# Performance work log

Hardware: AMD Instinct MI355X
Metric: run time of the kernel (lower is better)

The kernel has to match this reference:

```python
import jax, jax.numpy as jnp
import numpy as np

N = 50000          # nodes
E = 1600000        # edges (avg degree 32)
G = 256            # graphs in batch
IN_DIM = 128
HID = 64
NUM_LAYERS = 12    # stacked layers after the first
NUM_REL = 3
NEG_SLOPE = 0.2    # RGATConv default leaky_relu slope


def setup_inputs() -> dict:
    key = jax.random.key(0)
    ks = jax.random.split(key, 12)
    return {
        "node_features": jax.random.normal(ks[0], (N, IN_DIM), jnp.float32),
        "edge_index": jax.random.randint(ks[1], (2, E), 0, N, jnp.int32),
        "edge_type": jax.random.randint(ks[2], (E,), 0, NUM_REL, jnp.int32),
        "batch_index": jnp.sort(jax.random.randint(ks[3], (N,), 0, G, jnp.int32)),
        "W_first": jax.random.normal(ks[4], (NUM_REL, IN_DIM, HID), jnp.float32) / np.sqrt(IN_DIM).astype(np.float32),
        "q_first": jax.random.normal(ks[5], (HID,), jnp.float32) / np.sqrt(HID).astype(np.float32),
        "k_first": jax.random.normal(ks[6], (HID,), jnp.float32) / np.sqrt(HID).astype(np.float32),
        "b_first": jnp.zeros((HID,), jnp.float32),
        "W_stack": jax.random.normal(ks[7], (NUM_LAYERS, NUM_REL, HID, HID), jnp.float32) / np.sqrt(HID).astype(np.float32),
        "q_stack": jax.random.normal(ks[8], (NUM_LAYERS, HID), jnp.float32) / np.sqrt(HID).astype(np.float32),
        "k_stack": jax.random.normal(ks[9], (NUM_LAYERS, HID), jnp.float32) / np.sqrt(HID).astype(np.float32),
        "b_stack": jnp.zeros((NUM_LAYERS, HID), jnp.float32),
        "t": jnp.ones((1,), jnp.float32),
    }


def _segment_softmax(logits, seg, num_segments):
    # numerically-stable softmax over entries sharing a segment id (PyG `softmax`)
    m = jax.ops.segment_max(logits, seg, num_segments=num_segments)
    m = jnp.where(jnp.isfinite(m), m, 0.0)  # empty segments -> -inf, neutralize
    e = jnp.exp(logits - m[seg])
    s = jax.ops.segment_sum(e, seg, num_segments=num_segments)
    return e / (s[seg] + 1e-16)


def _rgat_layer(x, W, q, k, b, src, dst, etype):
    # PyG RGATConv, heads=1, dim=1, additive-self-attention, across-relation softmax.
    n = x.shape[0]
    xr = jnp.einsum('ni,rio->rno', x, W)       # [R,N,H] per-relation transform of all nodes
    qn = jnp.einsum('rno,o->rn', xr, q)        # [R,N] query scalar (out_i @ q)
    kn = jnp.einsum('rno,o->rn', xr, k)        # [R,N] key scalar   (out_j @ k)
    logits = jax.nn.leaky_relu(qn[etype, dst] + kn[etype, src], NEG_SLOPE)  # [E]
    alpha = _segment_softmax(logits, dst, n)   # softmax over incoming edges of each dst
    msg = alpha[:, None] * xr[etype, src]      # [E,H]
    return jax.ops.segment_sum(msg, dst, num_segments=n) + b


def reference(node_features, edge_index, edge_type, batch_index,
              W_first, q_first, k_first, b_first,
              W_stack, q_stack, k_stack, b_stack, t):
    src, dst = edge_index[0], edge_index[1]   # PyG convention: row=source j, col=target i
    x1 = _rgat_layer(node_features, W_first, q_first, k_first, b_first, src, dst, edge_type)

    def step(x, p):
        W, q, k, b = p
        y = _rgat_layer(x, W, q, k, b, src, dst, edge_type)
        return y, y

    _, ys = jax.lax.scan(step, x1, (W_stack, q_stack, k_stack, b_stack))
    all_x = jnp.concatenate([x1[None], ys], axis=0)                 # [13,N,H]
    node_rep = jnp.transpose(all_x, (1, 0, 2)).reshape(node_features.shape[0], -1)  # [N,13*H]

    # SoftmaxAggregation(learn=True): per-feature softmax over nodes of each graph
    alpha_g = _segment_softmax(node_rep * t[0], batch_index, G)     # [N,13*H]
    graph_rep = jax.ops.segment_sum(node_rep * alpha_g, batch_index, num_segments=G)
    return graph_rep, node_rep
```

## Files before the change

kernel.cpp:

```cpp
#include <hip/hip_runtime.h>
#include <math.h>

#define NN 50000
#define NE 1600000
#define NG 256
#define IND 128
#define HID 64
#define NREL 3
#define SLOPE 0.2f
#define XRS 192
#define NRS 832
#define WTP 136
#define W0SZ (192*128)
#define WLSZ (192*64)
#define WTOT (W0SZ + 12*WLSZ)
#define NBKT 49
#define ACHUNK 4096

typedef short bf16x8 __attribute__((ext_vector_type(8)));
typedef float f32x4 __attribute__((ext_vector_type(4)));

__device__ __forceinline__ float wred_max(float v){
  #pragma unroll
  for (int o = 32; o; o >>= 1) v = fmaxf(v, __shfl_xor(v, o));
  return v;
}
__device__ __forceinline__ float wred_sum(float v){
  #pragma unroll
  for (int o = 32; o; o >>= 1) v += __shfl_xor(v, o);
  return v;
}

__device__ __forceinline__ unsigned short f2bf(float f){
  unsigned int u = __float_as_uint(f);
  u = (u + 0x7FFFu + ((u >> 16) & 1u)) >> 16;
  return (unsigned short)u;
}
__device__ __forceinline__ float bf2f(unsigned short h){
  return __uint_as_float(((unsigned int)h) << 16);
}


__global__ __launch_bounds__(256) void bhistA_kernel(const int* __restrict__ dst,
                                                     int* __restrict__ bkt_cnt){
  __shared__ int h[64];
  int tid = threadIdx.x;
  if (tid < 64) h[tid] = 0;
  __syncthreads();
  int e0 = blockIdx.x * ACHUNK;
  int e1 = min(e0 + ACHUNK, NE);
  for (int i = e0 + tid; i < e1; i += 256)
    atomicAdd(&h[dst[i] >> 10], 1);
  __syncthreads();
  if (tid < 64 && h[tid] > 0) atomicAdd(&bkt_cnt[tid], h[tid]);
}

__global__ void bscan_kernel(const int* __restrict__ bkt_cnt, int* __restrict__ bkt_base,
                             int* __restrict__ bkt_fill, int* __restrict__ rowp){
  int tid = threadIdx.x;
  int v = (tid < NBKT) ? bkt_cnt[tid] : 0;
  int x = v;
  #pragma unroll
  for (int o = 1; o < 64; o <<= 1){ int t = __shfl_up(x, o); if (tid >= o) x += t; }
  int excl = x - v;
  if (tid <= NBKT){ bkt_base[tid] = excl; bkt_fill[tid] = excl; }
  if (tid == 0) rowp[NN] = NE;
}

__global__ __launch_bounds__(256) void bscatA_kernel(
    const int* __restrict__ src, const int* __restrict__ dst, const int* __restrict__ et,
    int* __restrict__ bkt_fill, unsigned int* __restrict__ ebkt){
  __shared__ int h[64];
  __shared__ int bbase[64];
  int tid = threadIdx.x;
  if (tid < 64) h[tid] = 0;
  __syncthreads();
  int e0 = blockIdx.x * ACHUNK;
  int e1 = min(e0 + ACHUNK, NE);
  for (int i = e0 + tid; i < e1; i += 256)
    atomicAdd(&h[dst[i] >> 10], 1);
  __syncthreads();
  if (tid < 64) bbase[tid] = (h[tid] > 0) ? atomicAdd(&bkt_fill[tid], h[tid]) : 0;
  __syncthreads();
  if (tid < 64) h[tid] = 0;
  __syncthreads();
  for (int i = e0 + tid; i < e1; i += 256){
    int d = dst[i];
    int b = d >> 10;
    int pos = atomicAdd(&h[b], 1);
    ebkt[bbase[b] + pos] =
        ((unsigned int)(d & 1023) << 18) | ((unsigned int)(et[i] & 3) << 16) | (unsigned int)src[i];
  }
}

__global__ __launch_bounds__(1024) void bsortB_kernel(
    const unsigned int* __restrict__ ebkt, const int* __restrict__ bkt_base,
    int* __restrict__ rowp, int* __restrict__ csr){
  __shared__ int cnt[1024];
  __shared__ int ws[16];
  int b = blockIdx.x, tid = threadIdx.x;
  int beg = bkt_base[b], end = bkt_base[b + 1];
  cnt[tid] = 0;
  __syncthreads();
  for (int i = beg + tid; i < end; i += 1024)
    atomicAdd(&cnt[(ebkt[i] >> 18) & 1023], 1);
  __syncthreads();
  int v = cnt[tid];
  int lane = tid & 63, wv = tid >> 6;
  int x = v;
  #pragma unroll
  for (int o = 1; o < 64; o <<= 1){ int t = __shfl_up(x, o); if (lane >= o) x += t; }
  if (lane == 63) ws[wv] = x;
  __syncthreads();
  if (tid < 16){
    int y = ws[tid];
    #pragma unroll
    for (int o = 1; o < 16; o <<= 1){ int t = __shfl_up(y, o); if (tid >= o) y += t; }
    ws[tid] = y;
  }
  __syncthreads();
  int excl = x + ((wv > 0) ? ws[wv - 1] : 0) - v;
  int node = b * 1024 + tid;
  if (node < NN) rowp[node] = beg + excl;
  cnt[tid] = excl;
  __syncthreads();
  for (int i = beg + tid; i < end; i += 1024){
    unsigned int p = ebkt[i];
    int dl = (p >> 18) & 1023;
    int pos = atomicAdd(&cnt[dl], 1);
    csr[beg + pos] = (int)(p & 0x3FFFFu);
  }
}

__global__ void gstart_kernel(const int* __restrict__ batch, int* __restrict__ gst){
  int n = blockIdx.x * blockDim.x + threadIdx.x;
  if (n > NN) return;
  int bc = (n < NN) ? batch[n] : NG;
  int bp = (n == 0) ? -1 : batch[n - 1];
  for (int g = bp + 1; g <= bc; ++g) gst[g] = n;
}

__global__ void wprep13_kernel(const float* __restrict__ Wf, const float* __restrict__ Ws,
                               unsigned short* __restrict__ Wtg13){
  int i = blockIdx.x * blockDim.x + threadIdx.x;
  if (i >= WTOT) return;
  int j, K; size_t base; const float* W;
  if (i < W0SZ){ j = i; K = IND; base = 0; W = Wf; }
  else {
    int t = i - W0SZ;
    int l = t / WLSZ;
    j = t - l * WLSZ; K = HID;
    base = W0SZ + (size_t)l * WLSZ;
    W = Ws + (size_t)l * WLSZ;
  }
  int h = j & 63;
  int k = (j >> 6) % K;
  int r = j / (K * HID);
  Wtg13[base + (size_t)((r << 6) + h) * K + k] = f2bf(W[j]);
}

__global__ __launch_bounds__(256) void mm_kernel(
    const float* __restrict__ x, int ldx, int K,
    const unsigned short* __restrict__ Wtg,
    const float* __restrict__ qv, const float* __restrict__ kv,
    unsigned short* __restrict__ XRb, float* __restrict__ QK){
  __shared__ unsigned short Wt[192 * WTP];
  int tid = threadIdx.x;
  int w = tid >> 6, lane = tid & 63;
  int lrow = lane & 15, kg = lane >> 4;
  int row0 = blockIdx.x * 64;
  int row = row0 + w * 16 + lrow;
  int nb8 = 192 * (K >> 3);
  for (int i = tid; i < nb8; i += 256){
    int col = i / (K >> 3);
    int k8 = (i - col * (K >> 3)) << 3;
    *(bf16x8*)&Wt[col * WTP + k8] = *(const bf16x8*)&Wtg[(size_t)col * K + k8];
  }
  __syncthreads();

  f32x4 acc[12];
  #pragma unroll
  for (int t = 0; t < 12; ++t) acc[t] = (f32x4){0.f, 0.f, 0.f, 0.f};

  int ksteps = K >> 5;
  for (int ks = 0; ks < ksteps; ++ks){
    bf16x8 xb;
    if (row < NN){
      const float* xp = x + (size_t)row * ldx + (ks << 5) + (kg << 3);
      float4 v0 = *(const float4*)xp;
      float4 v1 = *(const float4*)(xp + 4);
      xb[0] = (short)f2bf(v0.x); xb[1] = (short)f2bf(v0.y);
      xb[2] = (short)f2bf(v0.z); xb[3] = (short)f2bf(v0.w);
      xb[4] = (short)f2bf(v1.x); xb[5] = (short)f2bf(v1.y);
      xb[6] = (short)f2bf(v1.z); xb[7] = (short)f2bf(v1.w);
    } else {
      #pragma unroll
      for (int j = 0; j < 8; ++j) xb[j] = 0;
    }
    int kk = (ks << 5) + (kg << 3);
    #pragma unroll
    for (int t = 0; t < 12; ++t){
      bf16x8 wf = *(const bf16x8*)&Wt[(t * 16 + lrow) * WTP + kk];
      acc[t] = __builtin_amdgcn_mfma_f32_16x16x32_bf16(wf, xb, acc[t], 0, 0, 0);
    }
  }

  if (row < NN){
    unsigned short* orow = XRb + (size_t)row * XRS;
    #pragma unroll
    for (int t = 0; t < 12; ++t){
      ushort4 o4;
      o4.x = f2bf(acc[t][0]); o4.y = f2bf(acc[t][1]);
      o4.z = f2bf(acc[t][2]); o4.w = f2bf(acc[t][3]);
      *(ushort4*)(orow + t * 16 + (kg << 2)) = o4;
    }
  }

  float pq[3] = {0,0,0}, pk[3] = {0,0,0};
  #pragma unroll
  for (int t = 0; t < 12; ++t){
    int r = t >> 2;
    int hbase = ((t & 3) << 4) + (kg << 2);
    #pragma unroll
    for (int j = 0; j < 4; ++j){
      float qc = qv[hbase + j], kc = kv[hbase + j];
      pq[r] = fmaf(acc[t][j], qc, pq[r]);
      pk[r] = fmaf(acc[t][j], kc, pk[r]);
    }
  }
  #pragma unroll
  for (int o = 16; o < 64; o <<= 1){
    #pragma unroll
    for (int r = 0; r < 3; ++r){
      pq[r] += __shfl_xor(pq[r], o);
      pk[r] += __shfl_xor(pk[r], o);
    }
  }
  if (kg == 0 && row < NN){
    #pragma unroll
    for (int r = 0; r < 3; ++r){
      QK[row * 8 + r] = pq[r];
      QK[row * 8 + 3 + r] = pk[r];
    }
  }
}


__global__ __launch_bounds__(256) void edge_kernel(
    const unsigned short* __restrict__ XRb, const float* __restrict__ QK,
    const int* __restrict__ csr, const int* __restrict__ rowp,
    const float* __restrict__ bias, float* __restrict__ out){
  int wid = blockIdx.x * 4 + (threadIdx.x >> 6);
  int lane = threadIdx.x & 63;
  if (wid >= NN) return;
  int beg = rowp[wid], end = rowp[wid + 1];
  int cnt = end - beg;
  float* orow = out + (size_t)wid * NRS;
  int sub = lane & 7;
  int g   = lane >> 3;
  if (cnt == 0){
    if (lane < 8){
      float4 b0 = *(const float4*)(bias + sub * 8);
      float4 b1 = *(const float4*)(bias + sub * 8 + 4);
      *(float4*)(orow + sub * 8) = b0;
      *(float4*)(orow + sub * 8 + 4) = b1;
    }
    return;
  }
  float q0 = QK[wid * 8], q1 = QK[wid * 8 + 1], q2 = QK[wid * 8 + 2];

  if (cnt <= 128){
    float l0 = -INFINITY, l1 = -INFINITY;
    int o0 = 0, o1 = 0;
    {
      int idx = beg + lane;
      if (idx < end){
        int pk = csr[idx];
        int sn = pk & 0xFFFF, et = (pk >> 16) & 3;
        float lg = (et == 0 ? q0 : (et == 1 ? q1 : q2)) + QK[sn * 8 + 3 + et];
        l0 = lg >= 0.f ? lg : lg * SLOPE;
        o0 = sn * XRS + et * HID;
      }
      idx += 64;
      if (idx < end){
        int pk = csr[idx];
        int sn = pk & 0xFFFF, et = (pk >> 16) & 3;
        float lg = (et == 0 ? q0 : (et == 1 ? q1 : q2)) + QK[sn * 8 + 3 + et];
        l1 = lg >= 0.f ? lg : lg * SLOPE;
        o1 = sn * XRS + et * HID;
      }
    }
    float m = wred_max(fmaxf(l0, l1));
    float e0 = __expf(l0 - m), e1 = __expf(l1 - m);
    float s = wred_sum(e0 + e1);
    float inv = 1.f / (s + 1e-16f);
    float w0 = e0 * inv, w1 = e1 * inv;

    const unsigned short* xp = XRb + sub * 8;
    float acc[8] = {};

    float wS[8]; int oS[8];
    #pragma unroll
    for (int e = 0; e < 8; ++e){
      int sl = (e << 3) + g;
      wS[e] = __shfl(w0, sl);
      oS[e] = __shfl(o0, sl);
    }
    int nIt = (min(cnt, 64) + 7) >> 3;
    #pragma unroll
    for (int e = 0; e < 8; ++e){
      uint4 d = *(const uint4*)(xp + oS[e]);
      float we = wS[e];
      acc[0] = fmaf(we, __uint_as_float(d.x << 16), acc[0]);
      acc[1] = fmaf(we, __uint_as_float(d.x & 0xFFFF0000u), acc[1]);
      acc[2] = fmaf(we, __uint_as_float(d.y << 16), acc[2]);
      acc[3] = fmaf(we, __uint_as_float(d.y & 0xFFFF0000u), acc[3]);
      acc[4] = fmaf(we, __uint_as_float(d.z << 16), acc[4]);
      acc[5] = fmaf(we, __uint_as_float(d.z & 0xFFFF0000u), acc[5]);
      acc[6] = fmaf(we, __uint_as_float(d.w << 16), acc[6]);
      acc[7] = fmaf(we, __uint_as_float(d.w & 0xFFFF0000u), acc[7]);
      if (e + 1 >= nIt) break;
    }
    if (cnt > 64){
      #pragma unroll
      for (int e = 0; e < 8; ++e){
        int sl = (e << 3) + g;
        wS[e] = __shfl(w1, sl);
        oS[e] = __shfl(o1, sl);
      }
      int nIt2 = (cnt - 64 + 7) >> 3;
      #pragma unroll
      for (int e = 0; e < 8; ++e){
        uint4 d = *(const uint4*)(xp + oS[e]);
        float we = wS[e];
        acc[0] = fmaf(we, __uint_as_float(d.x << 16), acc[0]);
        acc[1] = fmaf(we, __uint_as_float(d.x & 0xFFFF0000u), acc[1]);
        acc[2] = fmaf(we, __uint_as_float(d.y << 16), acc[2]);
        acc[3] = fmaf(we, __uint_as_float(d.y & 0xFFFF0000u), acc[3]);
        acc[4] = fmaf(we, __uint_as_float(d.z << 16), acc[4]);
        acc[5] = fmaf(we, __uint_as_float(d.z & 0xFFFF0000u), acc[5]);
        acc[6] = fmaf(we, __uint_as_float(d.w << 16), acc[6]);
        acc[7] = fmaf(we, __uint_as_float(d.w & 0xFFFF0000u), acc[7]);
        if (e + 1 >= nIt2) break;
      }
    }
    #pragma unroll
    for (int o = 8; o < 64; o <<= 1)
      #pragma unroll
      for (int j = 0; j < 8; ++j)
        acc[j] += __shfl_xor(acc[j], o);
    if (lane < 8){
      float4 b0 = *(const float4*)(bias + sub * 8);
      float4 b1 = *(const float4*)(bias + sub * 8 + 4);
      float4 r0, r1;
      r0.x = acc[0] + b0.x; r0.y = acc[1] + b0.y; r0.z = acc[2] + b0.z; r0.w = acc[3] + b0.w;
      r1.x = acc[4] + b1.x; r1.y = acc[5] + b1.y; r1.z = acc[6] + b1.z; r1.w = acc[7] + b1.w;
      *(float4*)(orow + sub * 8) = r0;
      *(float4*)(orow + sub * 8 + 4) = r1;
    }
    return;
  }

  float bv = bias[lane];
  float m = -INFINITY, s = 0.f;
  for (int c = beg; c < end; c += 64){
    int idx = c + lane;
    float l = -INFINITY;
    if (idx < end){
      int pk = csr[idx];
      int sn = pk & 0xFFFF, et = (pk >> 16) & 3;
      float lg = (et == 0 ? q0 : (et == 1 ? q1 : q2)) + QK[sn * 8 + 3 + et];
      l = lg >= 0.f ? lg : lg * SLOPE;
    }
    float mnew = fmaxf(m, wred_max(l));
    float ps = wred_sum((idx < end) ? __expf(l - mnew) : 0.f);
    s = s * __expf(m - mnew) + ps;
    m = mnew;
  }
  float inv = 1.f / (s + 1e-16f);
  float acc = 0.f;
  for (int c = beg; c < end; c += 64){
    int idx = c + lane;
    int off = 0; float wgt = 0.f;
    if (idx < end){
      int pk = csr[idx];
      int sn = pk & 0xFFFF, et = (pk >> 16) & 3;
      float lg = (et == 0 ? q0 : (et == 1 ? q1 : q2)) + QK[sn * 8 + 3 + et];
      float l = lg >= 0.f ? lg : lg * SLOPE;
      wgt = __expf(l - m) * inv;
      off = sn * XRS + et * HID;
    }
    int cc = min(64, end - c);
    #pragma unroll 4
    for (int j = 0; j < cc; ++j){
      float wj = __uint_as_float(__builtin_amdgcn_readlane(__float_as_uint(wgt), j));
      int oj = __builtin_amdgcn_readlane(off, j);
      acc = fmaf(wj, bf2f(XRb[oj + lane]), acc);
    }
  }
  orow[lane] = acc + bv;
}

__global__ __launch_bounds__(256) void agg_kernel(
    const float* __restrict__ nr, const int* __restrict__ gst,
    const float* __restrict__ tp, float* __restrict__ out){
  __shared__ float rm[4][64], rs[4][64], ra[4][64];
  int g = blockIdx.x;
  int lane = threadIdx.x & 63;
  int w = threadIdx.x >> 6;
  int f = blockIdx.y * 64 + lane;
  int s = gst[g], e = gst[g + 1];
  float tval = tp[0];
  float m = -INFINITY, ss = 0.f, ac = 0.f;
  for (int n = s + w; n < e; n += 4){
    float v = nr[(size_t)n * NRS + f];
    float vm = v * tval;
    float Mn = fmaxf(m, vm);
    float sc = __expf(m - Mn);
    float ev = __expf(vm - Mn);
    ss = ss * sc + ev;
    ac = ac * sc + v * ev;
    m = Mn;
  }
  rm[w][lane] = m; rs[w][lane] = ss; ra[w][lane] = ac;
  __syncthreads();
  if (w == 0){
    float M = fmaxf(fmaxf(rm[0][lane], rm[1][lane]), fmaxf(rm[2][lane], rm[3][lane]));
    float S = 0.f, A = 0.f;
    #pragma unroll
    for (int i = 0; i < 4; ++i){
      float si = rs[i][lane];
      float sci = (si > 0.f) ? __expf(rm[i][lane] - M) : 0.f;
      S = fmaf(si, sci, S);
      A = fmaf(ra[i][lane], sci, A);
    }
    out[(size_t)g * NRS + f] = A / (S + 1e-16f);
  }
}


extern "C" void kernel_launch(void* const* d_in, const int* in_sizes, int n_in,
                              void* d_out, int out_size, void* d_ws, size_t ws_size,
                              hipStream_t stream){
  const float* x0   = (const float*)d_in[0];
  const int*   eidx = (const int*)d_in[1];
  const int*   etyp = (const int*)d_in[2];
  const int*   batch= (const int*)d_in[3];
  const float* Wf   = (const float*)d_in[4];
  const float* qf   = (const float*)d_in[5];
  const float* kf   = (const float*)d_in[6];
  const float* bf   = (const float*)d_in[7];
  const float* Ws   = (const float*)d_in[8];
  const float* qs   = (const float*)d_in[9];
  const float* ks   = (const float*)d_in[10];
  const float* bs   = (const float*)d_in[11];
  const float* tp   = (const float*)d_in[12];

  float* gout = (float*)d_out;
  float* nrep = gout + (size_t)NG * NRS;

  char* w = (char*)d_ws;
  unsigned short* XRb = (unsigned short*)w; w += (size_t)NN * XRS * 2;
  float* QK   = (float*)w;  w += (size_t)NN * 8 * 4;
  unsigned short* Wtg13 = (unsigned short*)w; w += (size_t)WTOT * 2;
  int*   rowp = (int*)w;    w += (size_t)(NN + 2) * 4;
  int*   gst  = (int*)w;    w += (size_t)(NG + 2) * 4;
  int*   bkt_cnt  = (int*)w; w += 64 * 4;
  int*   bkt_base = (int*)w; w += 64 * 4;
  int*   bkt_fill = (int*)w; w += 64 * 4;
  unsigned int* ebkt = (unsigned int*)w; w += (size_t)NE * 4;
  int*   csr  = (int*)w;    w += (size_t)NE * 4;

  const int* srcv = eidx;
  const int* dstv = eidx + NE;

  const int NAB = (NE + ACHUNK - 1) / ACHUNK;

  hipMemsetAsync(bkt_cnt, 0, 64 * 4, stream);
  bhistA_kernel<<<NAB, 256, 0, stream>>>(dstv, bkt_cnt);
  bscan_kernel<<<1, 64, 0, stream>>>(bkt_cnt, bkt_base, bkt_fill, rowp);
  bscatA_kernel<<<NAB, 256, 0, stream>>>(srcv, dstv, etyp, bkt_fill, ebkt);
  bsortB_kernel<<<NBKT, 1024, 0, stream>>>(ebkt, bkt_base, rowp, csr);
  gstart_kernel<<<(NN + 256) / 256, 256, 0, stream>>>(batch, gst);
  wprep13_kernel<<<(WTOT + 255) / 256, 256, 0, stream>>>(Wf, Ws, Wtg13);

  for (int l = 0; l < 13; ++l){
    int K = (l == 0) ? IND : HID;
    const unsigned short* Wtg = Wtg13 + ((l == 0) ? 0 : (W0SZ + (size_t)(l - 1) * WLSZ));
    const float* q  = (l == 0) ? qf : (qs + (size_t)(l - 1) * HID);
    const float* kv = (l == 0) ? kf : (ks + (size_t)(l - 1) * HID);
    const float* b  = (l == 0) ? bf : (bs + (size_t)(l - 1) * HID);
    const float* x  = (l == 0) ? x0 : (nrep + (size_t)(l - 1) * HID);
    int ldx = (l == 0) ? IND : NRS;
    mm_kernel<<<(NN + 63) / 64, 256, 0, stream>>>(x, ldx, K, Wtg, q, kv, XRb, QK);
    edge_kernel<<<(NN + 3) / 4, 256, 0, stream>>>(XRb, QK, csr, rowp, b, nrep + (size_t)l * HID);
  }
  dim3 ag(NG, 13);
  agg_kernel<<<ag, 256, 0, stream>>>(nrep, gst, tp, gout);
}
```

Before: 903.5 us.

## Emit bf16 copy of layer output and size mm shared memory per K

The edge kernel now also writes a compact bf16 copy of each node's layer output, and the next layer's matmul reads that copy instead of strided fp32 rows from the node representation. This halves the activation bytes the matmul reads and drops the per-step fp32 to bf16 conversion. The matmul's weight tile in shared memory is now dynamically sized to K+8 per row, so layers with K=64 reserve about half the LDS, which may allow more resident blocks. The cost is an extra bf16 store per node per layer in the edge kernel and one more workspace buffer.

```diff
diff --git a/kernel.cpp b/kernel.cpp
--- a/kernel.cpp
+++ b/kernel.cpp
@@ -10,7 +10,6 @@
 #define SLOPE 0.2f
 #define XRS 192
 #define NRS 832
-#define WTP 136
 #define W0SZ (192*128)
 #define WLSZ (192*64)
 #define WTOT (W0SZ + 12*WLSZ)
@@ -160,21 +159,23 @@
 }
 
 __global__ __launch_bounds__(256) void mm_kernel(
-    const float* __restrict__ x, int ldx, int K,
+    const float* __restrict__ xf, const unsigned short* __restrict__ xb,
+    int ldx, int K,
     const unsigned short* __restrict__ Wtg,
     const float* __restrict__ qv, const float* __restrict__ kv,
     unsigned short* __restrict__ XRb, float* __restrict__ QK){
-  __shared__ unsigned short Wt[192 * WTP];
+  extern __shared__ unsigned short Wt[];
+  int wtp = K + 8;
   int tid = threadIdx.x;
   int w = tid >> 6, lane = tid & 63;
   int lrow = lane & 15, kg = lane >> 4;
-  int row0 = blockIdx.x * 64;
-  int row = row0 + w * 16 + lrow;
-  int nb8 = 192 * (K >> 3);
+  int row = blockIdx.x * 64 + w * 16 + lrow;
+  int k8s = K >> 3;
+  int nb8 = 192 * k8s;
   for (int i = tid; i < nb8; i += 256){
-    int col = i / (K >> 3);
-    int k8 = (i - col * (K >> 3)) << 3;
-    *(bf16x8*)&Wt[col * WTP + k8] = *(const bf16x8*)&Wtg[(size_t)col * K + k8];
+    int col = i / k8s;
+    int k8 = (i - col * k8s) << 3;
+    *(bf16x8*)&Wt[col * wtp + k8] = *(const bf16x8*)&Wtg[(size_t)col * K + k8];
   }
   __syncthreads();
 
@@ -184,24 +185,27 @@
 
   int ksteps = K >> 5;
   for (int ks = 0; ks < ksteps; ++ks){
-    bf16x8 xb;
+    int kk = (ks << 5) + (kg << 3);
+    bf16x8 xv;
+    #pragma unroll
+    for (int j = 0; j < 8; ++j) xv[j] = 0;
     if (row < NN){
-      const float* xp = x + (size_t)row * ldx + (ks << 5) + (kg << 3);
-      float4 v0 = *(const float4*)xp;
-      float4 v1 = *(const float4*)(xp + 4);
-      xb[0] = (short)f2bf(v0.x); xb[1] = (short)f2bf(v0.y);
-      xb[2] = (short)f2bf(v0.z); xb[3] = (short)f2bf(v0.w);
-      xb[4] = (short)f2bf(v1.x); xb[5] = (short)f2bf(v1.y);
-      xb[6] = (short)f2bf(v1.z); xb[7] = (short)f2bf(v1.w);
-    } else {
-      #pragma unroll
-      for (int j = 0; j < 8; ++j) xb[j] = 0;
-    }
-    int kk = (ks << 5) + (kg << 3);
+      if (xb){
+        xv = *(const bf16x8*)(xb + (size_t)row * HID + kk);
+      } else {
+        const float* xp = xf + (size_t)row * ldx + kk;
+        float4 v0 = *(const float4*)xp;
+        float4 v1 = *(const float4*)(xp + 4);
+        xv[0] = (short)f2bf(v0.x); xv[1] = (short)f2bf(v0.y);
+        xv[2] = (short)f2bf(v0.z); xv[3] = (short)f2bf(v0.w);
+        xv[4] = (short)f2bf(v1.x); xv[5] = (short)f2bf(v1.y);
+        xv[6] = (short)f2bf(v1.z); xv[7] = (short)f2bf(v1.w);
+      }
+    }
     #pragma unroll
     for (int t = 0; t < 12; ++t){
-      bf16x8 wf = *(const bf16x8*)&Wt[(t * 16 + lrow) * WTP + kk];
-      acc[t] = __builtin_amdgcn_mfma_f32_16x16x32_bf16(wf, xb, acc[t], 0, 0, 0);
+      bf16x8 wf = *(const bf16x8*)&Wt[(t * 16 + lrow) * wtp + kk];
+      acc[t] = __builtin_amdgcn_mfma_f32_16x16x32_bf16(wf, xv, acc[t], 0, 0, 0);
     }
   }
 
@@ -249,13 +253,15 @@
 __global__ __launch_bounds__(256) void edge_kernel(
     const unsigned short* __restrict__ XRb, const float* __restrict__ QK,
     const int* __restrict__ csr, const int* __restrict__ rowp,
-    const float* __restrict__ bias, float* __restrict__ out){
+    const float* __restrict__ bias, float* __restrict__ out,
+    unsigned short* __restrict__ xb16){
   int wid = blockIdx.x * 4 + (threadIdx.x >> 6);
   int lane = threadIdx.x & 63;
   if (wid >= NN) return;
   int beg = rowp[wid], end = rowp[wid + 1];
   int cnt = end - beg;
   float* orow = out + (size_t)wid * NRS;
+  unsigned short* xrow = xb16 + (size_t)wid * HID;
   int sub = lane & 7;
   int g   = lane >> 3;
   if (cnt == 0){
@@ -264,6 +270,11 @@
       float4 b1 = *(const float4*)(bias + sub * 8 + 4);
       *(float4*)(orow + sub * 8) = b0;
       *(float4*)(orow + sub * 8 + 4) = b1;
+      ushort4 s0, s1;
+      s0.x = f2bf(b0.x); s0.y = f2bf(b0.y); s0.z = f2bf(b0.z); s0.w = f2bf(b0.w);
+      s1.x = f2bf(b1.x); s1.y = f2bf(b1.y); s1.z = f2bf(b1.z); s1.w = f2bf(b1.w);
+      *(ushort4*)(xrow + sub * 8) = s0;
+      *(ushort4*)(xrow + sub * 8 + 4) = s1;
     }
     return;
   }
@@ -357,6 +368,11 @@
       r1.x = acc[4] + b1.x; r1.y = acc[5] + b1.y; r1.z = acc[6] + b1.z; r1.w = acc[7] + b1.w;
       *(float4*)(orow + sub * 8) = r0;
       *(float4*)(orow + sub * 8 + 4) = r1;
+      ushort4 s0, s1;
+      s0.x = f2bf(r0.x); s0.y = f2bf(r0.y); s0.z = f2bf(r0.z); s0.w = f2bf(r0.w);
+      s1.x = f2bf(r1.x); s1.y = f2bf(r1.y); s1.z = f2bf(r1.z); s1.w = f2bf(r1.w);
+      *(ushort4*)(xrow + sub * 8) = s0;
+      *(ushort4*)(xrow + sub * 8 + 4) = s1;
     }
     return;
   }
@@ -398,7 +414,9 @@
       acc = fmaf(wj, bf2f(XRb[oj + lane]), acc);
     }
   }
-  orow[lane] = acc + bv;
+  float r = acc + bv;
+  orow[lane] = r;
+  xrow[lane] = f2bf(r);
 }
 
 __global__ __launch_bounds__(256) void agg_kernel(
@@ -461,6 +479,7 @@
 
   char* w = (char*)d_ws;
   unsigned short* XRb = (unsigned short*)w; w += (size_t)NN * XRS * 2;
+  unsigned short* xb16 = (unsigned short*)w; w += (size_t)NN * HID * 2;
   float* QK   = (float*)w;  w += (size_t)NN * 8 * 4;
   unsigned short* Wtg13 = (unsigned short*)w; w += (size_t)WTOT * 2;
   int*   rowp = (int*)w;    w += (size_t)(NN + 2) * 4;
@@ -476,7 +495,7 @@
 
   const int NAB = (NE + ACHUNK - 1) / ACHUNK;
 
-  hipMemsetAsync(bkt_cnt, 0, 64 * 4, stream);
+  (void)hipMemsetAsync(bkt_cnt, 0, 64 * 4, stream);
   bhistA_kernel<<<NAB, 256, 0, stream>>>(dstv, bkt_cnt);
   bscan_kernel<<<1, 64, 0, stream>>>(bkt_cnt, bkt_base, bkt_fill, rowp);
   bscatA_kernel<<<NAB, 256, 0, stream>>>(srcv, dstv, etyp, bkt_fill, ebkt);
@@ -490,10 +509,12 @@
     const float* q  = (l == 0) ? qf : (qs + (size_t)(l - 1) * HID);
     const float* kv = (l == 0) ? kf : (ks + (size_t)(l - 1) * HID);
     const float* b  = (l == 0) ? bf : (bs + (size_t)(l - 1) * HID);
-    const float* x  = (l == 0) ? x0 : (nrep + (size_t)(l - 1) * HID);
+    const float* xf = (l == 0) ? x0 : nullptr;
+    const unsigned short* xb = (l == 0) ? nullptr : xb16;
     int ldx = (l == 0) ? IND : NRS;
-    mm_kernel<<<(NN + 63) / 64, 256, 0, stream>>>(x, ldx, K, Wtg, q, kv, XRb, QK);
-    edge_kernel<<<(NN + 3) / 4, 256, 0, stream>>>(XRb, QK, csr, rowp, b, nrep + (size_t)l * HID);
+    size_t shb = (size_t)192 * (K + 8) * 2;
+    mm_kernel<<<(NN + 63) / 64, 256, shb, stream>>>(xf, xb, ldx, K, Wtg, q, kv, XRb, QK);
+    edge_kernel<<<(NN + 3) / 4, 256, 0, stream>>>(XRb, QK, csr, rowp, b, nrep + (size_t)l * HID, xb16);
   }
   dim3 ag(NG, 13);
   agg_kernel<<<ag, 256, 0, stream>>>(nrep, gst, tp, gout);
```

After: 926.1 us. 1.03x slower.
